# Kernel tuning notes

Measured on AMD Instinct MI355X. Metric: run time of the kernel, lower is better.

## Reference

```python
import jax, jax.numpy as jnp
import numpy as np

NUM_G = 16
OFFSET = jnp.linspace(0.0, 8.0, NUM_G)
COEFF = -0.5 / (8.0 / (NUM_G - 1)) ** 2  # GaussianSmearing coeff
EPS = 1e-5

N_NODES, N_EDGES, F_IN, HID, N_CLS, N_LAYERS = 20000, 320000, 6, 128, 21, 4


def _layernorm(h, g, b):
    m = jnp.mean(h, axis=-1, keepdims=True)
    v = jnp.var(h, axis=-1, keepdims=True)
    return (h - m) * jax.lax.rsqrt(v + EPS) * g + b


def setup_inputs() -> dict:
    key = jax.random.key(0)
    ks = jax.random.split(key, 16)
    Z = 2 * HID + NUM_G  # CGConv concat dim = 272

    def lin_w(k, shape, fan_in):
        lim = 1.0 / np.sqrt(fan_in)
        return jax.random.uniform(k, shape, jnp.float32, -lim, lim)

    return {
        "x": jax.random.normal(ks[0], (N_NODES, F_IN), jnp.float32),
        "edge_index": jax.random.randint(ks[1], (2, N_EDGES), 0, N_NODES, jnp.int32),
        "edge_dist": jax.random.uniform(ks[2], (N_EDGES,), jnp.float32, 0.0, 8.0),
        "W_node": lin_w(ks[3], (F_IN, HID), F_IN),
        "b_node": jnp.zeros((HID,), jnp.float32),
        "Wf": lin_w(ks[4], (N_LAYERS, Z, HID), Z),
        "bf": jnp.zeros((N_LAYERS, HID), jnp.float32),
        "Ws": lin_w(ks[5], (N_LAYERS, Z, HID), Z),
        "bs": jnp.zeros((N_LAYERS, HID), jnp.float32),
        "bn_g": jnp.ones((N_LAYERS, HID), jnp.float32),
        "bn_b": jnp.zeros((N_LAYERS, HID), jnp.float32),
        "ln_g": jnp.ones((N_LAYERS, HID), jnp.float32),
        "ln_b": jnp.zeros((N_LAYERS, HID), jnp.float32),
        "lnout_g": jnp.ones((HID,), jnp.float32),
        "lnout_b": jnp.zeros((HID,), jnp.float32),
        "W_fc": lin_w(ks[6], (HID, N_CLS), HID),
        "b_fc": jnp.zeros((N_CLS,), jnp.float32),
    }


def reference(x, edge_index, edge_dist, W_node, b_node, Wf, bf, Ws, bs,
              bn_g, bn_b, ln_g, ln_b, lnout_g, lnout_b, W_fc, b_fc):
    # edge RBF expansion: [E, 16]
    e = jnp.exp(COEFF * (edge_dist[:, None] - OFFSET[None, :]) ** 2)
    # node embedding: [N, H]
    h = x @ W_node + b_node
    src, dst = edge_index[0], edge_index[1]  # PyG: messages flow src (x_j) -> dst (x_i)
    n = h.shape[0]
    for l in range(Wf.shape[0]):
        # CGConv message: z = [x_i, x_j, e]; m = sigmoid(lin_f(z)) * softplus(lin_s(z))
        z = jnp.concatenate([h[dst], h[src], e], axis=-1)            # [E, 2H+16]
        msg = jax.nn.sigmoid(z @ Wf[l] + bf[l]) * jax.nn.softplus(z @ Ws[l] + bs[l])
        agg = jax.ops.segment_sum(msg, dst, num_segments=n)          # [N, H]
        # BatchNorm1d (training-mode batch stats) on aggregated messages
        mu = jnp.mean(agg, axis=0)
        var = jnp.var(agg, axis=0)
        agg = (agg - mu) * jax.lax.rsqrt(var + EPS) * bn_g[l] + bn_b[l]
        conv_out = agg + h                                           # CGConv residual
        # block: LayerNorm -> ReLU -> (dropout=identity in eval) -> + identity
        h = jax.nn.relu(_layernorm(conv_out, ln_g[l], ln_b[l])) + h
    h = _layernorm(h, lnout_g, lnout_b)
    return h @ W_fc + b_fc
```

## Files before the change

kernel.cpp:

```cpp
#include <hip/hip_runtime.h>
#include <hip/hip_fp16.h>
#include <math.h>

#define HID 128
#define NUMG 16
#define ZDIM 272
#define NCLS 21
#define LN_EPS 1e-5f
#define DELTA (8.0f/15.0f)
#define RBFC  (-1.7578125f)
#define NBINS 4096
#define LOG2E 1.44269504f
#define LN2F  0.69314718f

typedef _Float16 half8  __attribute__((ext_vector_type(8)));
typedef _Float16 half4t __attribute__((ext_vector_type(4)));
typedef float    floatx4 __attribute__((ext_vector_type(4)));

#if __has_builtin(__builtin_amdgcn_exp2f)
#define EXP2(x) __builtin_amdgcn_exp2f(x)
#else
#define EXP2(x) __expf(LN2F*(x))
#endif
#if __has_builtin(__builtin_amdgcn_logf)
#define LOG2(x) __builtin_amdgcn_logf(x)
#else
#define LOG2(x) (LOG2E*__logf(x))
#endif

__device__ __forceinline__ float frcp(float x){ return __builtin_amdgcn_rcpf(x); }

__launch_bounds__(256)
__global__ void preproc_kernel(const float* __restrict__ Wf, const float* __restrict__ Ws,
                               const float* __restrict__ bf, const float* __restrict__ bs,
                               _Float16* __restrict__ Wm16, float* __restrict__ Bias2,
                               _Float16* __restrict__ T,
                               const float* __restrict__ x, const float* __restrict__ Wn,
                               const float* __restrict__ bn, float* __restrict__ h,
                               const int* __restrict__ ei, int* __restrict__ deg,
                               int N, int E, int nhb){
  __shared__ float sW[16][256];
  __shared__ float sR[16][16];
  int b = blockIdx.x;
  int t = threadIdx.x;
  if (b < 1024){
    int idx = b*256 + t;
    {
      int l    = idx >> 16;
      int lane = (idx >> 3) & 63;
      int j    = idx & 7;
      int kb   = (idx >> 14) & 3;
      int tt   = (idx >> 9) & 31;
      int k    = kb*32 + ((lane >> 4) << 3) + j;
      int c    = tt*16 + (lane & 15);
      int row  = (c < 256) ? k : 128 + k;
      int cc   = (c < 256) ? c : c - 256;
      int f    = cc >> 1;
      const float* Wsel = ((c & 1) ? Ws : Wf) + l*ZDIM*HID;
      Wm16[idx] = (_Float16)Wsel[row*HID + f];
    }
    if (idx < 4*256){
      int l = idx >> 8; int c = idx & 255;
      Bias2[idx] = ((c & 1) ? bs : bf)[l*HID + (c >> 1)];
    }
  } else if (b < 2048){
    int bb   = b - 1024;
    int l    = bb >> 8;
    int bin0 = (bb & 255) * 16;
    for (int i = t; i < 16*256; i += 256){
      int k = i >> 8; int p = i & 255;
      int s = p & 1; int feat = (p >> 2) + ((p & 2) ? 64 : 0);
      const float* W = (s ? Ws : Wf) + l*ZDIM*HID;
      sW[k][p] = W[(256+k)*HID + feat];
    }
    {
      int bi = t >> 4; int k = t & 15;
      float d = 8.0f * (float)(bin0 + bi) / (float)(NBINS-1);
      float xx = d - (float)k * DELTA;
      sR[bi][k] = __expf(RBFC*xx*xx);
    }
    __syncthreads();
    for (int i = t; i < 16*256; i += 256){
      int bi = i >> 8; int p = i & 255;
      float acc = 0.f;
      #pragma unroll
      for (int k=0;k<16;k++) acc += sR[bi][k]*sW[k][p];
      T[((size_t)l*NBINS + bin0 + bi)*256 + p] = (_Float16)(acc*LOG2E);
    }
  } else if (b < 2048 + nhb){
    int idx = (b - 2048)*256 + t;
    if (idx < N*HID){
      int n = idx >> 7; int f = idx & 127;
      float acc = bn[f];
      const float* xr = x + n*6;
      #pragma unroll
      for (int k=0;k<6;k++) acc += xr[k]*Wn[k*HID+f];
      h[idx] = acc;
    }
  } else {
    int e = (b - 2048 - nhb)*256 + t;
    if (e < E) atomicAdd(&deg[ei[E + e]], 1);
  }
}


__global__ void scan_partial(const int* __restrict__ deg, int* __restrict__ bsum, int N){
  int t = threadIdx.x;
  int i = blockIdx.x*256 + t;
  int v = (i < N) ? deg[i] : 0;
  #pragma unroll
  for (int m=32;m;m>>=1) v += __shfl_xor(v, m, 64);
  __shared__ int ws[4];
  if ((t & 63) == 0) ws[t>>6] = v;
  __syncthreads();
  if (t == 0) bsum[blockIdx.x] = ws[0]+ws[1]+ws[2]+ws[3];
}

__global__ void scan_bsum(int* __restrict__ bsum, int nb){
  __shared__ int sm[256];
  int t = threadIdx.x;
  int v = (t < nb) ? bsum[t] : 0;
  sm[t] = v; __syncthreads();
  #pragma unroll
  for (int off=1; off<256; off<<=1){
    int add = (t >= off) ? sm[t-off] : 0;
    __syncthreads();
    sm[t] += add;
    __syncthreads();
  }
  if (t < nb) bsum[t] = sm[t] - v;
}

__global__ void scan_write(const int* __restrict__ deg, const int* __restrict__ bsum,
                           int* __restrict__ rowptr, int* __restrict__ cursor, int N, int E){
  __shared__ int sm[256];
  int t = threadIdx.x;
  int i = blockIdx.x*256 + t;
  int v = (i < N) ? deg[i] : 0;
  sm[t] = v; __syncthreads();
  #pragma unroll
  for (int off=1; off<256; off<<=1){
    int add = (t >= off) ? sm[t-off] : 0;
    __syncthreads();
    sm[t] += add;
    __syncthreads();
  }
  if (i < N){
    int ex = bsum[blockIdx.x] + sm[t] - v;
    rowptr[i] = ex; cursor[i] = ex;
  }
  if (i == 0) rowptr[N] = E;
}

__global__ void scatter_kernel(const int* __restrict__ ei, const float* __restrict__ dist,
                               int* __restrict__ cursor, int2* __restrict__ edata, int E){
  int e = blockIdx.x*256 + threadIdx.x;
  if (e >= E) return;
  int dst = ei[E + e];
  int pos = atomicAdd(&cursor[dst], 1);
  float d = dist[e];
  int b = (int)(d * ((float)(NBINS-1) / 8.0f) + 0.5f);
  if (b > NBINS-1) b = NBINS-1;
  if (b < 0) b = 0;
  edata[pos] = make_int2(ei[e]*256, b*256);
}


__launch_bounds__(256)
__global__ void node_gemm0_kernel(const float* __restrict__ h, const _Float16* __restrict__ Wm,
                                  const float* __restrict__ Bias2, _Float16* __restrict__ Pdst,
                                  _Float16* __restrict__ Psrc, float* __restrict__ bn_zero, int N){
  if (blockIdx.x == 0){ for (int i=threadIdx.x;i<1024;i+=256) bn_zero[i]=0.f; }
  int lane = threadIdx.x & 63;
  int w    = threadIdx.x >> 6;
  int m0   = blockIdx.x * 16;
  int arow = m0 + (lane & 15);
  int kbase= (lane >> 4) * 8;
  floatx4 acc[8];
  #pragma unroll
  for (int t=0;t<8;t++) acc[t] = (floatx4){0.f,0.f,0.f,0.f};
  #pragma unroll
  for (int kb=0; kb<4; kb++){
    const float* ap = h + arow*HID + kb*32 + kbase;
    float4 a0 = *(const float4*)ap;
    float4 a1 = *(const float4*)(ap+4);
    half8 af;
    af[0]=(_Float16)a0.x; af[1]=(_Float16)a0.y; af[2]=(_Float16)a0.z; af[3]=(_Float16)a0.w;
    af[4]=(_Float16)a1.x; af[5]=(_Float16)a1.y; af[6]=(_Float16)a1.z; af[7]=(_Float16)a1.w;
    const _Float16* bp = Wm + ((kb*32 + w*8)*64 + lane)*8;
    #pragma unroll
    for (int t=0;t<8;t++){
      half8 b8 = *(const half8*)(bp + t*512);
      acc[t] = __builtin_amdgcn_mfma_f32_16x16x32_f16(af, b8, acc[t], 0,0,0);
    }
  }
  int quad = lane >> 4;
  int cl   = lane & 15;
  int hi2  = (w & 1) ? 2 : 0;
  if (w < 2){
    #pragma unroll
    for (int t=0;t<8;t++){
      int cp = t*16 + cl;
      int c  = (w&1)*128 + cp;
      int p  = ((cp >> 1) << 2) + hi2 + (cp & 1);
      float b2 = Bias2[c];
      #pragma unroll
      for (int r=0;r<4;r++)
        Pdst[(m0 + quad*4 + r)*256 + p] = (_Float16)((acc[t][r] + b2)*LOG2E);
    }
  } else {
    #pragma unroll
    for (int t=0;t<8;t++){
      int cp = t*16 + cl;
      int p  = ((cp >> 1) << 2) + hi2 + (cp & 1);
      #pragma unroll
      for (int r=0;r<4;r++)
        Psrc[(m0 + quad*4 + r)*256 + p] = (_Float16)(acc[t][r]*LOG2E);
    }
  }
}

__launch_bounds__(256)
__global__ void fused_apply_gemm(const float2* __restrict__ agg2, float* __restrict__ h,
                                 const float* __restrict__ bn_in, float* __restrict__ bn_zero,
                                 const float* __restrict__ bng, const float* __restrict__ bnb,
                                 const float* __restrict__ lng, const float* __restrict__ lnb,
                                 float invN,
                                 const _Float16* __restrict__ Wm, const float* __restrict__ Bias2,
                                 _Float16* __restrict__ Pdst, _Float16* __restrict__ Psrc, int N){
  __shared__ float sh[16][132];
  int t = threadIdx.x;
  if (blockIdx.x == 0){ for (int i=t;i<1024;i+=256) bn_zero[i]=0.f; }
  int lane = t & 63, w = t >> 6;
  int f0 = lane, f1 = lane + 64;
  float sm0=0.f,sq0=0.f,sm1=0.f,sq1=0.f;
  #pragma unroll
  for (int s=0;s<4;s++){
    sm0 += bn_in[s*256 + 2*lane];
    sm1 += bn_in[s*256 + 2*lane + 1];
    sq0 += bn_in[s*256 + 128 + 2*lane];
    sq1 += bn_in[s*256 + 129 + 2*lane];
  }
  float mu0 = sm0*invN, mu1 = sm1*invN;
  float rv0 = rsqrtf(sq0*invN - mu0*mu0 + LN_EPS);
  float rv1 = rsqrtf(sq1*invN - mu1*mu1 + LN_EPS);
  float G0 = bng[f0], B0 = bnb[f0], G1 = bng[f1], B1 = bnb[f1];
  float Lg0 = lng[f0], Lb0 = lnb[f0], Lg1 = lng[f1], Lb1 = lnb[f1];
  int row0 = blockIdx.x*16;
  #pragma unroll
  for (int i=0;i<4;i++){
    int rr = w*4 + i; int row = row0 + rr;
    float2 a = agg2[row*64 + lane];
    float h0 = h[row*HID + f0], h1 = h[row*HID + f1];
    float c0 = (a.x - mu0)*rv0*G0 + B0 + h0;
    float c1 = (a.y - mu1)*rv1*G1 + B1 + h1;
    float s = c0 + c1, q = c0*c0 + c1*c1;
    #pragma unroll
    for (int m=32;m;m>>=1){ s += __shfl_xor(s,m,64); q += __shfl_xor(q,m,64); }
    float mean = s*(1.0f/128.0f);
    float var  = q*(1.0f/128.0f) - mean*mean;
    float r = rsqrtf(var + LN_EPS);
    float n0 = fmaxf((c0-mean)*r*Lg0 + Lb0, 0.f) + h0;
    float n1 = fmaxf((c1-mean)*r*Lg1 + Lb1, 0.f) + h1;
    h[row*HID + f0] = n0; h[row*HID + f1] = n1;
    sh[rr][f0] = n0; sh[rr][f1] = n1;
  }
  __syncthreads();
  int arl  = lane & 15;
  int kbase= (lane >> 4) * 8;
  floatx4 acc[8];
  #pragma unroll
  for (int k=0;k<8;k++) acc[k] = (floatx4){0.f,0.f,0.f,0.f};
  #pragma unroll
  for (int kb=0; kb<4; kb++){
    const float* ap = &sh[arl][kb*32 + kbase];
    float4 a0 = *(const float4*)ap;
    float4 a1 = *(const float4*)(ap+4);
    half8 af;
    af[0]=(_Float16)a0.x; af[1]=(_Float16)a0.y; af[2]=(_Float16)a0.z; af[3]=(_Float16)a0.w;
    af[4]=(_Float16)a1.x; af[5]=(_Float16)a1.y; af[6]=(_Float16)a1.z; af[7]=(_Float16)a1.w;
    const _Float16* bp = Wm + ((kb*32 + w*8)*64 + lane)*8;
    #pragma unroll
    for (int k=0;k<8;k++){
      half8 b8 = *(const half8*)(bp + k*512);
      acc[k] = __builtin_amdgcn_mfma_f32_16x16x32_f16(af, b8, acc[k], 0,0,0);
    }
  }
  int quad = lane >> 4;
  int cl   = lane & 15;
  int hi2  = (w & 1) ? 2 : 0;
  int m0   = row0;
  if (w < 2){
    #pragma unroll
    for (int k=0;k<8;k++){
      int cp = k*16 + cl;
      int c  = (w&1)*128 + cp;
      int p  = ((cp >> 1) << 2) + hi2 + (cp & 1);
      float b2 = Bias2[c];
      #pragma unroll
      for (int r=0;r<4;r++)
        Pdst[(m0 + quad*4 + r)*256 + p] = (_Float16)((acc[k][r] + b2)*LOG2E);
    }
  } else {
    #pragma unroll
    for (int k=0;k<8;k++){
      int cp = k*16 + cl;
      int p  = ((cp >> 1) << 2) + hi2 + (cp & 1);
      #pragma unroll
      for (int r=0;r<4;r++)
        Psrc[(m0 + quad*4 + r)*256 + p] = (_Float16)(acc[k][r]*LOG2E);
    }
  }
}

__launch_bounds__(256)
__global__ void agg_kernel(const _Float16* __restrict__ Pdst, const _Float16* __restrict__ Psrc,
                           const int2* __restrict__ edata, const int* __restrict__ rowptr,
                           const _Float16* __restrict__ T,
                           float2* __restrict__ agg2){
  int lane = threadIdx.x & 63;
  int w    = threadIdx.x >> 6;
  int half = lane >> 5;
  int hl   = lane & 31;
  int l8   = hl * 8;
  int node = blockIdx.x*4 + w;
  half8 ad8 = *(const half8*)(Pdst + node*256 + l8);
  floatx4 acc = (floatx4){0.f,0.f,0.f,0.f};
  int beg = rowptr[node], end = rowptr[node+1];
  int len  = end - beg;
  int len0 = (len + 1) >> 1;
  int s = beg + half*len0;
  int e = half ? end : (beg + len0);

  auto body = [&](half8 p8, half8 t8, float vm){
    half8 z = p8 + ad8 + t8;
    float xf0=(float)z[0], xs0=(float)z[1], xf1=(float)z[2], xs1=(float)z[3];
    float xf2=(float)z[4], xs2=(float)z[5], xf3=(float)z[6], xs3=(float)z[7];
    float g0  = vm*frcp(1.f + EXP2(-xf0));
    float sp0 = fmaxf(xs0, 0.f) + LOG2(1.f + EXP2(-fabsf(xs0)));
    float g1  = vm*frcp(1.f + EXP2(-xf1));
    float sp1 = fmaxf(xs1, 0.f) + LOG2(1.f + EXP2(-fabsf(xs1)));
    float g2  = vm*frcp(1.f + EXP2(-xf2));
    float sp2 = fmaxf(xs2, 0.f) + LOG2(1.f + EXP2(-fabsf(xs2)));
    float g3  = vm*frcp(1.f + EXP2(-xf3));
    float sp3 = fmaxf(xs3, 0.f) + LOG2(1.f + EXP2(-fabsf(xs3)));
    acc[0] = fmaf(g0, sp0, acc[0]);
    acc[1] = fmaf(g1, sp1, acc[1]);
    acc[2] = fmaf(g2, sp2, acc[2]);
    acc[3] = fmaf(g3, sp3, acc[3]);
  };

  for (int j0 = s; j0 < e; j0 += 4){
    int j1 = j0+1 < e ? j0+1 : e-1;
    int j2 = j0+2 < e ? j0+2 : e-1;
    int j3 = j0+3 < e ? j0+3 : e-1;
    int2 ed0 = edata[j0], ed1 = edata[j1], ed2 = edata[j2], ed3 = edata[j3];
    half8 p0 = *(const half8*)(Psrc + ed0.x + l8);
    half8 t0 = *(const half8*)(T    + ed0.y + l8);
    half8 p1 = *(const half8*)(Psrc + ed1.x + l8);
    half8 t1 = *(const half8*)(T    + ed1.y + l8);
    half8 p2 = *(const half8*)(Psrc + ed2.x + l8);
    half8 t2 = *(const half8*)(T    + ed2.y + l8);
    half8 p3 = *(const half8*)(Psrc + ed3.x + l8);
    half8 t3 = *(const half8*)(T    + ed3.y + l8);
    body(p0, t0, 1.f);
    body(p1, t1, (j0+1 < e) ? 1.f : 0.f);
    body(p2, t2, (j0+2 < e) ? 1.f : 0.f);
    body(p3, t3, (j0+3 < e) ? 1.f : 0.f);
  }
  #pragma unroll
  for (int c=0;c<4;c++) acc[c] += __shfl_xor(acc[c], 32, 64);
  int col = (hl << 1) | half;
  float2 outv = half ? make_float2(acc[2]*LN2F, acc[3]*LN2F)
                     : make_float2(acc[0]*LN2F, acc[1]*LN2F);
  agg2[node*64 + col] = outv;
}

__global__ void bnstats_kernel(const float* __restrict__ agg, float* __restrict__ bnstat, int N){
  int f = threadIdx.x;
  float s = 0.f, q = 0.f;
  for (int r = blockIdx.x; r < N; r += gridDim.x){
    float v = agg[r*HID + f];
    s += v; q += v*v;
  }
  float* sb = bnstat + ((blockIdx.x & 3) << 8);
  atomicAdd(sb + f,       s);
  atomicAdd(sb + 128 + f, q);
}

__launch_bounds__(256)
__global__ void lnfc_kernel(const float2* __restrict__ agg2, const float* __restrict__ h,
                            const float* __restrict__ bn_in,
                            const float* __restrict__ bng, const float* __restrict__ bnb,
                            const float* __restrict__ lng, const float* __restrict__ lnb,
                            float invN,
                            const float* __restrict__ g, const float* __restrict__ b,
                            const float* __restrict__ Wfc, const float* __restrict__ bfc,
                            float* __restrict__ out, int N){
  __shared__ float sh[16][132];
  __shared__ float wl[HID*NCLS];
  __shared__ float bl[NCLS];
  int t = threadIdx.x;
  for (int i = t; i < HID*NCLS; i += 256) wl[i] = Wfc[i];
  if (t < NCLS) bl[t] = bfc[t];
  int lane = t & 63, w = t >> 6;
  int f0 = lane, f1 = lane + 64;
  float sm0=0.f,sq0=0.f,sm1=0.f,sq1=0.f;
  #pragma unroll
  for (int s=0;s<4;s++){
    sm0 += bn_in[s*256 + 2*lane];
    sm1 += bn_in[s*256 + 2*lane + 1];
    sq0 += bn_in[s*256 + 128 + 2*lane];
    sq1 += bn_in[s*256 + 129 + 2*lane];
  }
  float mu0 = sm0*invN, mu1 = sm1*invN;
  float rv0 = rsqrtf(sq0*invN - mu0*mu0 + LN_EPS);
  float rv1 = rsqrtf(sq1*invN - mu1*mu1 + LN_EPS);
  float G0 = bng[f0], B0 = bnb[f0], G1 = bng[f1], B1 = bnb[f1];
  float Lg0 = lng[f0], Lb0 = lnb[f0], Lg1 = lng[f1], Lb1 = lnb[f1];
  float Fg0 = g[f0], Fb0 = b[f0], Fg1 = g[f1], Fb1 = b[f1];
  int row0 = blockIdx.x*16;
  #pragma unroll
  for (int i=0;i<4;i++){
    int rr = w*4 + i; int row = row0 + rr;
    float2 a = agg2[row*64 + lane];
    float h0 = h[row*HID + f0], h1 = h[row*HID + f1];
    float c0 = (a.x - mu0)*rv0*G0 + B0 + h0;
    float c1 = (a.y - mu1)*rv1*G1 + B1 + h1;
    float s = c0 + c1, q = c0*c0 + c1*c1;
    #pragma unroll
    for (int m=32;m;m>>=1){ s += __shfl_xor(s,m,64); q += __shfl_xor(q,m,64); }
    float mean = s*(1.0f/128.0f);
    float var  = q*(1.0f/128.0f) - mean*mean;
    float r = rsqrtf(var + LN_EPS);
    float n0 = fmaxf((c0-mean)*r*Lg0 + Lb0, 0.f) + h0;
    float n1 = fmaxf((c1-mean)*r*Lg1 + Lb1, 0.f) + h1;
    float s2 = n0 + n1, q2 = n0*n0 + n1*n1;
    #pragma unroll
    for (int m=32;m;m>>=1){ s2 += __shfl_xor(s2,m,64); q2 += __shfl_xor(q2,m,64); }
    float mean2 = s2*(1.0f/128.0f);
    float var2  = q2*(1.0f/128.0f) - mean2*mean2;
    float r2 = rsqrtf(var2 + LN_EPS);
    sh[rr][f0] = (n0-mean2)*r2*Fg0 + Fb0;
    sh[rr][f1] = (n1-mean2)*r2*Fg1 + Fb1;
  }
  __syncthreads();
  for (int idx = t; idx < 16*NCLS; idx += 256){
    int r = idx / NCLS, c = idx - r*NCLS;
    int orow = row0 + r;
    if (orow < N){
      float acc = bl[c];
      #pragma unroll 4
      for (int k=0;k<HID;k++) acc += sh[r][k]*wl[k*NCLS + c];
      out[orow*NCLS + c] = acc;
    }
  }
}


extern "C" void kernel_launch(void* const* d_in, const int* in_sizes, int n_in,
                              void* d_out, int out_size, void* d_ws, size_t ws_size,
                              hipStream_t stream){
  const float* x    = (const float*)d_in[0];
  const int*   ei   = (const int*)  d_in[1];
  const float* dist = (const float*)d_in[2];
  const float* Wn   = (const float*)d_in[3];
  const float* bn   = (const float*)d_in[4];
  const float* Wf   = (const float*)d_in[5];
  const float* bf   = (const float*)d_in[6];
  const float* Ws   = (const float*)d_in[7];
  const float* bs   = (const float*)d_in[8];
  const float* bng  = (const float*)d_in[9];
  const float* bnb  = (const float*)d_in[10];
  const float* lng  = (const float*)d_in[11];
  const float* lnb  = (const float*)d_in[12];
  const float* lnog = (const float*)d_in[13];
  const float* lnob = (const float*)d_in[14];
  const float* Wfc  = (const float*)d_in[15];
  const float* bfc  = (const float*)d_in[16];
  float* out = (float*)d_out;

  const int N = in_sizes[0] / 6;
  const int E = in_sizes[2];
  const int NB = (N + 255)/256;
  const int nhb = (N*HID + 255)/256;
  const int neb = (E + 255)/256;

  char* p = (char*)d_ws;
  auto alloc = [&](size_t bytes)->void*{
    void* r = (void*)p;
    p += (bytes + 255) & ~(size_t)255;
    return r;
  };
  float*     h      = (float*)    alloc((size_t)N*HID*4);
  _Float16*  Pdst   = (_Float16*) alloc((size_t)N*256*2);
  _Float16*  Psrc   = (_Float16*) alloc((size_t)N*256*2);
  float2*    agg2   = (float2*)   alloc((size_t)N*64*8);
  _Float16*  Wm16   = (_Float16*) alloc((size_t)4*65536*2);
  float*     Bias2  = (float*)    alloc((size_t)4*256*4);
  _Float16*  T      = (_Float16*) alloc((size_t)4*NBINS*256*2);
  float*     bnstat = (float*)    alloc((size_t)2*1024*4);
  int*       deg    = (int*)      alloc((size_t)N*4);
  int*       rowptr = (int*)      alloc((size_t)(N+1)*4);
  int*       cursor = (int*)      alloc((size_t)N*4);
  int*       bsum   = (int*)      alloc((size_t)NB*4);
  int2*      edata  = (int2*)     alloc((size_t)E*8);

  hipMemsetAsync(deg, 0, (size_t)N*4, stream);
  preproc_kernel<<<2048 + nhb + neb, 256, 0, stream>>>(
      Wf, Ws, bf, bs, Wm16, Bias2, T, x, Wn, bn, h, ei, deg, N, E, nhb);
  scan_partial<<<NB, 256, 0, stream>>>(deg, bsum, N);
  scan_bsum<<<1, 256, 0, stream>>>(bsum, NB);
  scan_write<<<NB, 256, 0, stream>>>(deg, bsum, rowptr, cursor, N, E);
  scatter_kernel<<<neb, 256, 0, stream>>>(ei, dist, cursor, edata, E);

  float invN = 1.0f / (float)N;

  node_gemm0_kernel<<<N/16, 256, 0, stream>>>(
      h, Wm16, Bias2, Pdst, Psrc, bnstat, N);
  agg_kernel<<<N/4, 256, 0, stream>>>(
      Pdst, Psrc, edata, rowptr, T, agg2);
  bnstats_kernel<<<1024, 128, 0, stream>>>((const float*)agg2, bnstat, N);

  for (int l = 1; l < 4; l++){
    float* bn_in   = bnstat + ((l-1)&1)*1024;
    float* bn_next = bnstat + (l&1)*1024;
    fused_apply_gemm<<<N/16, 256, 0, stream>>>(
        agg2, h, bn_in, bn_next,
        bng + (l-1)*HID, bnb + (l-1)*HID, lng + (l-1)*HID, lnb + (l-1)*HID, invN,
        Wm16 + (size_t)l*65536, Bias2 + (size_t)l*256, Pdst, Psrc, N);
    agg_kernel<<<N/4, 256, 0, stream>>>(
        Pdst, Psrc, edata, rowptr, T + (size_t)l*NBINS*256, agg2);
    bnstats_kernel<<<1024, 128, 0, stream>>>((const float*)agg2, bn_next, N);
  }

  lnfc_kernel<<<N/16, 256, 0, stream>>>(
      agg2, h, bnstat + 1024,
      bng + 3*HID, bnb + 3*HID, lng + 3*HID, lnb + 3*HID, invN,
      lnog, lnob, Wfc, bfc, out, N);
}
```

Measured before the change: 416.1 us.

## Fuse BatchNorm stats into aggregation and replace three-pass scan with atomic-base CSR

Removes the separate bnstats kernel by having each agg_kernel block reduce its outputs' sums and squares in shared memory and atomically add them into one of 16 sharded stat buffers. This avoids re-reading the whole aggregated tensor four times, at the cost of more atomics per layer. It also collapses the three-kernel prefix scan into a single kernel that takes each block's base offset from an atomic counter. Because that counter hands out bases in arbitrary order, rowptr is no longer monotonic, so agg_kernel now uses deg for the segment length instead of rowptr[node+1].

```diff
diff --git a/kernel.cpp b/kernel.cpp
--- a/kernel.cpp
+++ b/kernel.cpp
@@ -12,9 +12,9 @@
 #define NBINS 4096
 #define LOG2E 1.44269504f
 #define LN2F  0.69314718f
+#define NSHARD 16
 
 typedef _Float16 half8  __attribute__((ext_vector_type(8)));
-typedef _Float16 half4t __attribute__((ext_vector_type(4)));
 typedef float    floatx4 __attribute__((ext_vector_type(4)));
 
 #if __has_builtin(__builtin_amdgcn_exp2f)
@@ -103,23 +103,13 @@
   }
 }
 
-
-__global__ void scan_partial(const int* __restrict__ deg, int* __restrict__ bsum, int N){
+__global__ void csr_kernel(const int* __restrict__ deg, int* __restrict__ rowptr,
+                           int* __restrict__ cursor, int* __restrict__ gbase, int N){
+  __shared__ int sm[256];
+  __shared__ int base;
   int t = threadIdx.x;
   int i = blockIdx.x*256 + t;
   int v = (i < N) ? deg[i] : 0;
-  #pragma unroll
-  for (int m=32;m;m>>=1) v += __shfl_xor(v, m, 64);
-  __shared__ int ws[4];
-  if ((t & 63) == 0) ws[t>>6] = v;
-  __syncthreads();
-  if (t == 0) bsum[blockIdx.x] = ws[0]+ws[1]+ws[2]+ws[3];
-}
-
-__global__ void scan_bsum(int* __restrict__ bsum, int nb){
-  __shared__ int sm[256];
-  int t = threadIdx.x;
-  int v = (t < nb) ? bsum[t] : 0;
   sm[t] = v; __syncthreads();
   #pragma unroll
   for (int off=1; off<256; off<<=1){
@@ -128,28 +118,12 @@
     sm[t] += add;
     __syncthreads();
   }
-  if (t < nb) bsum[t] = sm[t] - v;
-}
-
-__global__ void scan_write(const int* __restrict__ deg, const int* __restrict__ bsum,
-                           int* __restrict__ rowptr, int* __restrict__ cursor, int N, int E){
-  __shared__ int sm[256];
-  int t = threadIdx.x;
-  int i = blockIdx.x*256 + t;
-  int v = (i < N) ? deg[i] : 0;
-  sm[t] = v; __syncthreads();
-  #pragma unroll
-  for (int off=1; off<256; off<<=1){
-    int add = (t >= off) ? sm[t-off] : 0;
-    __syncthreads();
-    sm[t] += add;
-    __syncthreads();
-  }
+  if (t == 255) base = atomicAdd(gbase, sm[255]);
+  __syncthreads();
   if (i < N){
-    int ex = bsum[blockIdx.x] + sm[t] - v;
+    int ex = base + sm[t] - v;
     rowptr[i] = ex; cursor[i] = ex;
   }
-  if (i == 0) rowptr[N] = E;
 }
 
 __global__ void scatter_kernel(const int* __restrict__ ei, const float* __restrict__ dist,
@@ -170,7 +144,7 @@
 __global__ void node_gemm0_kernel(const float* __restrict__ h, const _Float16* __restrict__ Wm,
                                   const float* __restrict__ Bias2, _Float16* __restrict__ Pdst,
                                   _Float16* __restrict__ Psrc, float* __restrict__ bn_zero, int N){
-  if (blockIdx.x == 0){ for (int i=threadIdx.x;i<1024;i+=256) bn_zero[i]=0.f; }
+  if (blockIdx.x == 0){ for (int i=threadIdx.x;i<NSHARD*256;i+=256) bn_zero[i]=0.f; }
   int lane = threadIdx.x & 63;
   int w    = threadIdx.x >> 6;
   int m0   = blockIdx.x * 16;
@@ -230,12 +204,12 @@
                                  _Float16* __restrict__ Pdst, _Float16* __restrict__ Psrc, int N){
   __shared__ float sh[16][132];
   int t = threadIdx.x;
-  if (blockIdx.x == 0){ for (int i=t;i<1024;i+=256) bn_zero[i]=0.f; }
+  if (blockIdx.x == 0){ for (int i=t;i<NSHARD*256;i+=256) bn_zero[i]=0.f; }
   int lane = t & 63, w = t >> 6;
   int f0 = lane, f1 = lane + 64;
   float sm0=0.f,sq0=0.f,sm1=0.f,sq1=0.f;
   #pragma unroll
-  for (int s=0;s<4;s++){
+  for (int s=0;s<NSHARD;s++){
     sm0 += bn_in[s*256 + 2*lane];
     sm1 += bn_in[s*256 + 2*lane + 1];
     sq0 += bn_in[s*256 + 128 + 2*lane];
@@ -316,8 +290,10 @@
 __launch_bounds__(256)
 __global__ void agg_kernel(const _Float16* __restrict__ Pdst, const _Float16* __restrict__ Psrc,
                            const int2* __restrict__ edata, const int* __restrict__ rowptr,
+                           const int* __restrict__ deg,
                            const _Float16* __restrict__ T,
-                           float2* __restrict__ agg2){
+                           float2* __restrict__ agg2, float* __restrict__ bnstat){
+  __shared__ float sred[4][64][4];
   int lane = threadIdx.x & 63;
   int w    = threadIdx.x >> 6;
   int half = lane >> 5;
@@ -326,8 +302,9 @@
   int node = blockIdx.x*4 + w;
   half8 ad8 = *(const half8*)(Pdst + node*256 + l8);
   floatx4 acc = (floatx4){0.f,0.f,0.f,0.f};
-  int beg = rowptr[node], end = rowptr[node+1];
-  int len  = end - beg;
+  int beg = rowptr[node];
+  int len = deg[node];
+  int end = beg + len;
   int len0 = (len + 1) >> 1;
   int s = beg + half*len0;
   int e = half ? end : (beg + len0);
@@ -374,18 +351,17 @@
   float2 outv = half ? make_float2(acc[2]*LN2F, acc[3]*LN2F)
                      : make_float2(acc[0]*LN2F, acc[1]*LN2F);
   agg2[node*64 + col] = outv;
-}
-
-__global__ void bnstats_kernel(const float* __restrict__ agg, float* __restrict__ bnstat, int N){
-  int f = threadIdx.x;
-  float s = 0.f, q = 0.f;
-  for (int r = blockIdx.x; r < N; r += gridDim.x){
-    float v = agg[r*HID + f];
-    s += v; q += v*v;
-  }
-  float* sb = bnstat + ((blockIdx.x & 3) << 8);
-  atomicAdd(sb + f,       s);
-  atomicAdd(sb + 128 + f, q);
+  sred[w][col][0] = outv.x;
+  sred[w][col][1] = outv.y;
+  sred[w][col][2] = outv.x*outv.x;
+  sred[w][col][3] = outv.y*outv.y;
+  __syncthreads();
+  int t = threadIdx.x;
+  int c = t & 63, part = t >> 6;
+  float sum = sred[0][c][part] + sred[1][c][part] + sred[2][c][part] + sred[3][c][part];
+  float* sb = bnstat + ((blockIdx.x & (NSHARD-1)) << 8);
+  int idx = ((part >> 1) * 128) + 2*c + (part & 1);
+  atomicAdd(sb + idx, sum);
 }
 
 __launch_bounds__(256)
@@ -407,7 +383,7 @@
   int f0 = lane, f1 = lane + 64;
   float sm0=0.f,sq0=0.f,sm1=0.f,sq1=0.f;
   #pragma unroll
-  for (int s=0;s<4;s++){
+  for (int s=0;s<NSHARD;s++){
     sm0 += bn_in[s*256 + 2*lane];
     sm1 += bn_in[s*256 + 2*lane + 1];
     sq0 += bn_in[s*256 + 128 + 2*lane];
@@ -499,19 +475,16 @@
   _Float16*  Wm16   = (_Float16*) alloc((size_t)4*65536*2);
   float*     Bias2  = (float*)    alloc((size_t)4*256*4);
   _Float16*  T      = (_Float16*) alloc((size_t)4*NBINS*256*2);
-  float*     bnstat = (float*)    alloc((size_t)2*1024*4);
-  int*       deg    = (int*)      alloc((size_t)N*4);
-  int*       rowptr = (int*)      alloc((size_t)(N+1)*4);
+  float*     bnstat = (float*)    alloc((size_t)2*NSHARD*256*4);
+  int*       deg    = (int*)      alloc((size_t)(N+1)*4);
+  int*       rowptr = (int*)      alloc((size_t)N*4);
   int*       cursor = (int*)      alloc((size_t)N*4);
-  int*       bsum   = (int*)      alloc((size_t)NB*4);
   int2*      edata  = (int2*)     alloc((size_t)E*8);
 
-  hipMemsetAsync(deg, 0, (size_t)N*4, stream);
+  hipMemsetAsync(deg, 0, (size_t)(N+1)*4, stream);
   preproc_kernel<<<2048 + nhb + neb, 256, 0, stream>>>(
       Wf, Ws, bf, bs, Wm16, Bias2, T, x, Wn, bn, h, ei, deg, N, E, nhb);
-  scan_partial<<<NB, 256, 0, stream>>>(deg, bsum, N);
-  scan_bsum<<<1, 256, 0, stream>>>(bsum, NB);
-  scan_write<<<NB, 256, 0, stream>>>(deg, bsum, rowptr, cursor, N, E);
+  csr_kernel<<<NB, 256, 0, stream>>>(deg, rowptr, cursor, deg + N, N);
   scatter_kernel<<<neb, 256, 0, stream>>>(ei, dist, cursor, edata, E);
 
   float invN = 1.0f / (float)N;
@@ -519,23 +492,21 @@
   node_gemm0_kernel<<<N/16, 256, 0, stream>>>(
       h, Wm16, Bias2, Pdst, Psrc, bnstat, N);
   agg_kernel<<<N/4, 256, 0, stream>>>(
-      Pdst, Psrc, edata, rowptr, T, agg2);
-  bnstats_kernel<<<1024, 128, 0, stream>>>((const float*)agg2, bnstat, N);
+      Pdst, Psrc, edata, rowptr, deg, T, agg2, bnstat);
 
   for (int l = 1; l < 4; l++){
-    float* bn_in   = bnstat + ((l-1)&1)*1024;
-    float* bn_next = bnstat + (l&1)*1024;
+    float* bn_in   = bnstat + ((l-1)&1)*NSHARD*256;
+    float* bn_next = bnstat + (l&1)*NSHARD*256;
     fused_apply_gemm<<<N/16, 256, 0, stream>>>(
         agg2, h, bn_in, bn_next,
         bng + (l-1)*HID, bnb + (l-1)*HID, lng + (l-1)*HID, lnb + (l-1)*HID, invN,
         Wm16 + (size_t)l*65536, Bias2 + (size_t)l*256, Pdst, Psrc, N);
     agg_kernel<<<N/4, 256, 0, stream>>>(
-        Pdst, Psrc, edata, rowptr, T + (size_t)l*NBINS*256, agg2);
-    bnstats_kernel<<<1024, 128, 0, stream>>>((const float*)agg2, bn_next, N);
+        Pdst, Psrc, edata, rowptr, deg, T + (size_t)l*NBINS*256, agg2, bn_next);
   }
 
   lnfc_kernel<<<N/16, 256, 0, stream>>>(
-      agg2, h, bnstat + 1024,
+      agg2, h, bnstat + NSHARD*256,
       bng + 3*HID, bnb + 3*HID, lng + 3*HID, lnb + 3*HID, invN,
       lnog, lnob, Wfc, bfc, out, N);
 }
```

Result: faster. 394.1 us (-5.3%).
